# Kernel optimization log

Measured on AMD Instinct MI355X. Metric: run time of the kernel, lower is better.

Reference implementation:

```python
import jax, jax.numpy as jnp
import numpy as np

QMIN, QMAX = -128, 127  # signed int8 range


def setup_inputs() -> dict:
    key = jax.random.key(0)
    k_x, k_w, k_b = jax.random.split(key, 3)
    N, C_in, H, W = 32, 128, 56, 56
    C_out, kH, kW = 256, 3, 3
    # int8-valued tensors carried as int32 (jax-friendly); values in [-128, 127]
    x = jax.random.randint(k_x, (N, C_in, H, W), 0, 256, dtype=jnp.int32) - 128
    weight = jax.random.randint(k_w, (C_out, C_in, kH, kW), 0, 256, dtype=jnp.int32) - 128
    # int32 bias, already quantized with scale s_in * s_w
    bias = jax.random.randint(k_b, (C_out,), -(2 ** 14), 2 ** 14, dtype=jnp.int32)
    return {
        "x": x,
        "weight": weight,
        "bias": bias,
        "input_scale": jnp.float32(0.02),
        "weight_scale": jnp.float32(0.005),
        "output_scale": jnp.float32(0.05),
        "input_zero_point": jnp.int32(-5),
        "output_zero_point": jnp.int32(3),
    }


def reference(x, weight, bias, input_scale, weight_scale, output_scale,
              input_zero_point, output_zero_point):
    # Dequant-style integer conv: shift input by its zero point (weights are
    # symmetric, zero point 0), accumulate in fp32 (stands in for int32 acc).
    x_f = (x - input_zero_point).astype(jnp.float32)
    w_f = weight.astype(jnp.float32)
    acc = jax.lax.conv_general_dilated(
        x_f, w_f,
        window_strides=(1, 1),
        padding=((1, 1), (1, 1)),
        dimension_numbers=("NCHW", "OIHW", "NCHW"),
    )
    acc = acc + bias.astype(jnp.float32)[None, :, None, None]
    # Requantize: scale fusion + output zero point, round, clamp to int8.
    requant_scale = input_scale * weight_scale / output_scale
    y = acc * requant_scale + output_zero_point.astype(jnp.float32)
    y_q = jnp.clip(jnp.round(y), QMIN, QMAX).astype(jnp.int8)
    return y_q
```

## Files before the change

kernel.cpp:

```cpp
#include <hip/hip_runtime.h>
#include <stdint.h>


#define NB 32
#define CI 128
#define HH 56
#define WW 56
#define CO 256
#define SPA (HH * WW)
#define HP 58
#define WP 64
#define XP2_BYTES (NB * HP * WP * CI)
#define BP_BYTES (9 * 2 * 4 * CO * 16)

typedef int v4i __attribute__((ext_vector_type(4)));

__global__ __launch_bounds__(256) void prep_kernel(
    const int* __restrict__ x, const int* __restrict__ wgt,
    const int* __restrict__ bias, const int* __restrict__ zpi,
    int8_t* __restrict__ xp2, int8_t* __restrict__ bp, int* __restrict__ BG)
{
    __shared__ int sm[1824];
    const int tid = threadIdx.x, bid = blockIdx.x;
    const int zp = *zpi;
    const int zp4 = (zp & 255) * 0x01010101;

    if (bid < HH * NB) {
        const int n = bid / HH, h = bid % HH;
        #pragma unroll
        for (int it = 0; it < 7; ++it) {
            int j = tid + it * 256;
            int ci = j / 14, w4 = j - ci * 14;
            const v4i v = *(const v4i*)(x + ((n * CI + ci) * HH + h) * WW + w4 * 4);
            sm[w4 * 130 + ci] = (v.x & 255) | ((v.y & 255) << 8) |
                                ((v.z & 255) << 16) | (v.w << 24);
        }
        __syncthreads();
        int* od = (int*)xp2 + (n * HP + h + 1) * (WP * CI / 4);
        #pragma unroll
        for (int it = 0; it < 8; ++it) {
            int j = tid + it * 256;
            int widx = j >> 5, ci4 = j & 31;
            int val = zp4;
            if (widx >= 1 && widx <= WW) {
                int w = widx - 1;
                int base = (w >> 2) * 130 + ci4 * 4;
                int sh = (w & 3) * 8;
                val = ((sm[base] >> sh) & 0xff) | (((sm[base+1] >> sh) & 0xff) << 8) |
                      (((sm[base+2] >> sh) & 0xff) << 16) | ((sm[base+3] >> sh) << 24);
            }
            od[j ^ ((widx & 7) << 2)] = val;
        }
    } else if (bid < HH * NB + 2 * NB) {
        const int z = bid - HH * NB;
        const int n = z >> 1, hidx = (z & 1) ? (HP - 1) : 0;
        int* od = (int*)xp2 + (n * HP + hidx) * (WP * CI / 4);
        #pragma unroll
        for (int it = 0; it < 8; ++it) od[tid + it * 256] = zp4;
    } else {
        const int co = bid - (HH * NB + 2 * NB);
        for (int j = tid; j < 1152; j += 256) sm[j] = wgt[co * 1152 + j];
        __syncthreads();
        for (int j = tid; j < 288; j += 256) {
            int j4 = j & 3, q = (j >> 2) & 3, c64 = (j >> 4) & 1, t = j >> 5;
            int ci = c64 * 64 + q * 16 + j4 * 4;
            int b0 = sm[(ci + 0) * 9 + t] & 255, b1 = sm[(ci + 1) * 9 + t] & 255;
            int b2 = sm[(ci + 2) * 9 + t] & 255, b3 = sm[(ci + 3) * 9 + t];
            ((int*)bp)[((t * 2 + c64) * 4 + q) * 1024 + co * 4 + j4] =
                b0 | (b1 << 8) | (b2 << 16) | (b3 << 24);
        }
        if (tid < 9) {
            int s = 0;
            for (int ci = 0; ci < CI; ++ci) s += sm[ci * 9 + tid];
            sm[1152 + tid] = s;
        }
        __syncthreads();
        if (tid == 0) {
            int s9 = 0;
            for (int t = 0; t < 9; ++t) s9 += sm[1152 + t];
            BG[co] = bias[co] - zp * s9;
        }
    }
}

__global__ __launch_bounds__(256, 1) void qconv_mfma(
    const int8_t* __restrict__ xp2, const int8_t* __restrict__ bp,
    const int* __restrict__ BG,
    const float* __restrict__ si, const float* __restrict__ sw,
    const float* __restrict__ so, const int* __restrict__ zpo,
    int* __restrict__ out)
{
    const int tid  = threadIdx.x, lane = tid & 63, wid = tid >> 6;
    const int quad = lane >> 4, lo16 = lane & 15;
    const int bid  = blockIdx.x;
    const int x    = bid & 7, yb = bid >> 3;
    const int half = yb >> 4, coli = yb & 15;
    const int col  = x * 16 + coli;
    const int n = col >> 2, co64 = col & 3;
    const int cobase = co64 * 64;
    const int sfirst = half;
    const int ntiles = half ? 3 : 4;

    __shared__ __attribute__((aligned(16))) char smem[152 * 1024];
    char* Asm = smem;
    char* Bsm = smem + 80 * 1024;

    #pragma unroll
    for (int k = 0; k < 18; ++k) {
        const int u = wid + 4 * k;
        __builtin_amdgcn_global_load_lds(
            (const __attribute__((address_space(1))) void*)(bp + (u << 12) + cobase * 16 + lane * 16),
            (__attribute__((address_space(3))) void*)(Bsm + (u << 10)), 16, 0, 0);
    }
    const int8_t* aslab0 = xp2 + (((size_t)n * HP + sfirst * 8) << 13);
    #pragma unroll
    for (int k = 0; k < 20; ++k) {
        const int u = wid + 4 * k;
        __builtin_amdgcn_global_load_lds(
            (const __attribute__((address_space(1))) void*)(aslab0 + (u << 10) + lane * 16),
            (__attribute__((address_space(3))) void*)(Asm + (u << 10)), 16, 0, 0);
    }

    int abase[7];
    const int mw = wid * 112;
    #pragma unroll
    for (int mt = 0; mt < 7; ++mt) {
        const int ml = mw + mt * 16 + lo16;
        const int srow = ml / 56, scol = ml - srow * 56;
        abase[mt] = (srow * WP + scol) * 128 + quad * 16;
    }

    int bgv[4];
    #pragma unroll
    for (int ct = 0; ct < 4; ++ct) bgv[ct] = BG[cobase + ct * 16 + lo16];
    const float rs = (*si) * (*sw) / (*so);
    const float zo = (float)(*zpo);

    int* optr = out + (n * CO + cobase + lo16) * SPA + mw + quad * 4;

    __syncthreads();

    for (int tile = 0; tile < ntiles; ++tile) {
        const int slab = sfirst + 2 * tile;
        const int havenext = (tile + 1 < ntiles);

        v4i pre[20];
        if (havenext) {
            const int8_t* anext = xp2 + (((size_t)n * HP + (slab + 2) * 8) << 13);
            #pragma unroll
            for (int i = 0; i < 20; ++i)
                pre[i] = *(const v4i*)(anext + i * 4096 + tid * 16);
        }

        v4i acc[7][4];
        #pragma unroll
        for (int mt = 0; mt < 7; ++mt)
            #pragma unroll
            for (int ct = 0; ct < 4; ++ct) acc[mt][ct] = (v4i){0, 0, 0, 0};

        #pragma unroll
        for (int t = 0; t < 9; ++t) {
            const int toff = ((t / 3) * WP + (t % 3)) * 128;
            v4i b[2][4];
            #pragma unroll
            for (int c = 0; c < 2; ++c)
                #pragma unroll
                for (int ct = 0; ct < 4; ++ct)
                    b[c][ct] = *(const v4i*)(Bsm + ((t * 2 + c) * 4 + quad) * 1024 +
                                             lo16 * 16 + ct * 256);
            #pragma unroll
            for (int mt = 0; mt < 7; ++mt) {
                const int P = abase[mt] + toff;
                const int phys = P ^ (((P >> 7) & 7) << 4);
                v4i a0 = *(const v4i*)(Asm + phys);
                v4i a1 = *(const v4i*)(Asm + (phys ^ 64));
                #pragma unroll
                for (int ct = 0; ct < 4; ++ct)
                    acc[mt][ct] = __builtin_amdgcn_mfma_i32_16x16x64_i8(a0, b[0][ct], acc[mt][ct], 0, 0, 0);
                #pragma unroll
                for (int ct = 0; ct < 4; ++ct)
                    acc[mt][ct] = __builtin_amdgcn_mfma_i32_16x16x64_i8(a1, b[1][ct], acc[mt][ct], 0, 0, 0);
            }
        }

        __builtin_amdgcn_sched_barrier(0);
        __builtin_amdgcn_s_barrier();
        __builtin_amdgcn_sched_barrier(0);

        if (havenext) {
            #pragma unroll
            for (int i = 0; i < 20; ++i)
                *(v4i*)(Asm + i * 4096 + tid * 16) = pre[i];
        }

        const int sbase = slab * 448;
        #pragma unroll
        for (int mt = 0; mt < 7; ++mt) {
            #pragma unroll
            for (int ct = 0; ct < 4; ++ct) {
                v4i vv;
                #pragma unroll
                for (int i = 0; i < 4; ++i) {
                    float yv = rintf((float)(acc[mt][ct][i] + bgv[ct]) * rs + zo);
                    yv = fminf(fmaxf(yv, -128.f), 127.f);
                    vv[i] = (int)yv;
                }
                *(v4i*)(optr + sbase + ct * 16 * SPA + mt * 16) = vv;
            }
        }

        if (havenext) {
            asm volatile("s_waitcnt lgkmcnt(0)" ::: "memory");
            __builtin_amdgcn_sched_barrier(0);
            __builtin_amdgcn_s_barrier();
            __builtin_amdgcn_sched_barrier(0);
        }
    }
}

extern "C" void kernel_launch(void* const* d_in, const int* in_sizes, int n_in,
                              void* d_out, int out_size, void* d_ws, size_t ws_size,
                              hipStream_t stream) {
    const int*   x    = (const int*)d_in[0];
    const int*   wgt  = (const int*)d_in[1];
    const int*   bias = (const int*)d_in[2];
    const float* si   = (const float*)d_in[3];
    const float* sw   = (const float*)d_in[4];
    const float* so   = (const float*)d_in[5];
    const int*   zpi  = (const int*)d_in[6];
    const int*   zpo  = (const int*)d_in[7];
    int* out = (int*)d_out;

    int8_t* xp2 = (int8_t*)d_ws;
    int8_t* bp  = xp2 + XP2_BYTES;
    int*    bg  = (int*)(bp + BP_BYTES);

    prep_kernel<<<HH * NB + 2 * NB + CO, 256, 0, stream>>>(x, wgt, bias, zpi, xp2, bp, bg);
    qconv_mfma<<<256, 256, 0, stream>>>(xp2, bp, bg, si, sw, so, zpo, out);
}
```

Measured before the change: 196.8 us.

## Keep weights in registers, shrink A tiles, double-buffer LDS with async loads

Restructures the conv kernel so each wave keeps its 32-channel weight fragments resident in registers instead of re-reading them from LDS every tile. The workgroup splits into a 2x2 grid over spatial rows and output channels. It now processes seven 4-row slabs with a double-buffered LDS A tile, prefetched through global_load_lds, replacing register staging plus LDS stores. This removes LDS traffic for B and the register-to-LDS copy. The cost is heavy VGPR use (144 regs for weights) and a hand-tuned vmcnt wait whose correctness depends on the in-flight load count.

```diff
diff --git a/kernel.cpp b/kernel.cpp
--- a/kernel.cpp
+++ b/kernel.cpp
@@ -12,6 +12,7 @@
 #define WP 64
 #define XP2_BYTES (NB * HP * WP * CI)
 #define BP_BYTES (9 * 2 * 4 * CO * 16)
+#define ABUF (6 * 8192)
 
 typedef int v4i __attribute__((ext_vector_type(4)));
 
@@ -93,111 +94,99 @@
     const int tid  = threadIdx.x, lane = tid & 63, wid = tid >> 6;
     const int quad = lane >> 4, lo16 = lane & 15;
     const int bid  = blockIdx.x;
-    const int x    = bid & 7, yb = bid >> 3;
-    const int half = yb >> 4, coli = yb & 15;
-    const int col  = x * 16 + coli;
-    const int n = col >> 2, co64 = col & 3;
-    const int cobase = co64 * 64;
-    const int sfirst = half;
-    const int ntiles = half ? 3 : 4;
-
-    __shared__ __attribute__((aligned(16))) char smem[152 * 1024];
-    char* Asm = smem;
-    char* Bsm = smem + 80 * 1024;
-
-    #pragma unroll
-    for (int k = 0; k < 18; ++k) {
+    const int x    = bid & 7, r = bid >> 3;
+    const int n    = x * 4 + (r & 3);
+    const int co64 = (r >> 2) & 3;
+    const int p    = r >> 4;
+    const int mh   = wid >> 1, ch = wid & 1;
+    const int cw   = co64 * 64 + ch * 32;
+
+    __shared__ __attribute__((aligned(16))) int8_t Asm[2][ABUF];
+
+    const int8_t* src0 = xp2 + (((size_t)n * HP + 4 * p) << 13);
+    #pragma unroll
+    for (int k = 0; k < 12; ++k) {
         const int u = wid + 4 * k;
         __builtin_amdgcn_global_load_lds(
-            (const __attribute__((address_space(1))) void*)(bp + (u << 12) + cobase * 16 + lane * 16),
-            (__attribute__((address_space(3))) void*)(Bsm + (u << 10)), 16, 0, 0);
-    }
-    const int8_t* aslab0 = xp2 + (((size_t)n * HP + sfirst * 8) << 13);
-    #pragma unroll
-    for (int k = 0; k < 20; ++k) {
-        const int u = wid + 4 * k;
-        __builtin_amdgcn_global_load_lds(
-            (const __attribute__((address_space(1))) void*)(aslab0 + (u << 10) + lane * 16),
-            (__attribute__((address_space(3))) void*)(Asm + (u << 10)), 16, 0, 0);
-    }
-
-    int abase[7];
-    const int mw = wid * 112;
-    #pragma unroll
-    for (int mt = 0; mt < 7; ++mt) {
-        const int ml = mw + mt * 16 + lo16;
-        const int srow = ml / 56, scol = ml - srow * 56;
-        abase[mt] = (srow * WP + scol) * 128 + quad * 16;
-    }
-
-    int bgv[4];
-    #pragma unroll
-    for (int ct = 0; ct < 4; ++ct) bgv[ct] = BG[cobase + ct * 16 + lo16];
+            (const __attribute__((address_space(1))) void*)(src0 + (u << 10) + lane * 16),
+            (__attribute__((address_space(3))) void*)(&Asm[0][u << 10]), 16, 0, 0);
+    }
+
+    v4i breg[9][2][2];
+    #pragma unroll
+    for (int t = 0; t < 9; ++t)
+        #pragma unroll
+        for (int c = 0; c < 2; ++c)
+            #pragma unroll
+            for (int ct = 0; ct < 2; ++ct)
+                breg[t][c][ct] = *(const v4i*)(bp + (((t * 2 + c) * 4 + quad) << 12) +
+                                               (cw + ct * 16 + lo16) * 16);
+
+    int bgv[2];
+    #pragma unroll
+    for (int ct = 0; ct < 2; ++ct) bgv[ct] = BG[cw + ct * 16 + lo16];
     const float rs = (*si) * (*sw) / (*so);
     const float zo = (float)(*zpo);
 
-    int* optr = out + (n * CO + cobase + lo16) * SPA + mw + quad * 4;
+    int rowoff[7], colp[7][3];
+    #pragma unroll
+    for (int mt = 0; mt < 7; ++mt) {
+        const int ml = mh * 112 + mt * 16 + lo16;
+        const int srow = ml / 56, scol = ml - srow * 56;
+        rowoff[mt] = srow * 8192;
+        #pragma unroll
+        for (int dc = 0; dc < 3; ++dc) {
+            const int c2 = scol + dc;
+            colp[mt][dc] = (c2 * 128 + quad * 16) ^ ((c2 & 7) << 4);
+        }
+    }
 
     __syncthreads();
 
-    for (int tile = 0; tile < ntiles; ++tile) {
-        const int slab = sfirst + 2 * tile;
-        const int havenext = (tile + 1 < ntiles);
-
-        v4i pre[20];
-        if (havenext) {
-            const int8_t* anext = xp2 + (((size_t)n * HP + (slab + 2) * 8) << 13);
-            #pragma unroll
-            for (int i = 0; i < 20; ++i)
-                pre[i] = *(const v4i*)(anext + i * 4096 + tid * 16);
-        }
-
-        v4i acc[7][4];
+    #pragma unroll 1
+    for (int t7 = 0; t7 < 7; ++t7) {
+        const int s = p + 2 * t7;
+        const int8_t* curA = Asm[t7 & 1];
+
+        if (t7 < 6) {
+            const int8_t* srcn = xp2 + (((size_t)n * HP + 4 * (s + 2)) << 13);
+            int8_t* dst = (int8_t*)Asm[(t7 & 1) ^ 1];
+            #pragma unroll
+            for (int k = 0; k < 12; ++k) {
+                const int u = wid + 4 * k;
+                __builtin_amdgcn_global_load_lds(
+                    (const __attribute__((address_space(1))) void*)(srcn + (u << 10) + lane * 16),
+                    (__attribute__((address_space(3))) void*)(dst + (u << 10)), 16, 0, 0);
+            }
+        }
+        __builtin_amdgcn_sched_barrier(0);
+
+        v4i acc[7][2];
         #pragma unroll
         for (int mt = 0; mt < 7; ++mt)
             #pragma unroll
-            for (int ct = 0; ct < 4; ++ct) acc[mt][ct] = (v4i){0, 0, 0, 0};
-
-        #pragma unroll
-        for (int t = 0; t < 9; ++t) {
-            const int toff = ((t / 3) * WP + (t % 3)) * 128;
-            v4i b[2][4];
-            #pragma unroll
-            for (int c = 0; c < 2; ++c)
-                #pragma unroll
-                for (int ct = 0; ct < 4; ++ct)
-                    b[c][ct] = *(const v4i*)(Bsm + ((t * 2 + c) * 4 + quad) * 1024 +
-                                             lo16 * 16 + ct * 256);
+            for (int ct = 0; ct < 2; ++ct) acc[mt][ct] = (v4i){0, 0, 0, 0};
+
+        #pragma unroll
+        for (int tp = 0; tp < 9; ++tp) {
+            const int dr = tp / 3, dc = tp % 3;
             #pragma unroll
             for (int mt = 0; mt < 7; ++mt) {
-                const int P = abase[mt] + toff;
-                const int phys = P ^ (((P >> 7) & 7) << 4);
-                v4i a0 = *(const v4i*)(Asm + phys);
-                v4i a1 = *(const v4i*)(Asm + (phys ^ 64));
-                #pragma unroll
-                for (int ct = 0; ct < 4; ++ct)
-                    acc[mt][ct] = __builtin_amdgcn_mfma_i32_16x16x64_i8(a0, b[0][ct], acc[mt][ct], 0, 0, 0);
-                #pragma unroll
-                for (int ct = 0; ct < 4; ++ct)
-                    acc[mt][ct] = __builtin_amdgcn_mfma_i32_16x16x64_i8(a1, b[1][ct], acc[mt][ct], 0, 0, 0);
-            }
-        }
-
-        __builtin_amdgcn_sched_barrier(0);
-        __builtin_amdgcn_s_barrier();
-        __builtin_amdgcn_sched_barrier(0);
-
-        if (havenext) {
-            #pragma unroll
-            for (int i = 0; i < 20; ++i)
-                *(v4i*)(Asm + i * 4096 + tid * 16) = pre[i];
-        }
-
-        const int sbase = slab * 448;
+                const int off = rowoff[mt] + dr * 8192 + colp[mt][dc];
+                v4i a0 = *(const v4i*)(curA + off);
+                v4i a1 = *(const v4i*)(curA + (off ^ 64));
+                acc[mt][0] = __builtin_amdgcn_mfma_i32_16x16x64_i8(a0, breg[tp][0][0], acc[mt][0], 0, 0, 0);
+                acc[mt][1] = __builtin_amdgcn_mfma_i32_16x16x64_i8(a0, breg[tp][0][1], acc[mt][1], 0, 0, 0);
+                acc[mt][0] = __builtin_amdgcn_mfma_i32_16x16x64_i8(a1, breg[tp][1][0], acc[mt][0], 0, 0, 0);
+                acc[mt][1] = __builtin_amdgcn_mfma_i32_16x16x64_i8(a1, breg[tp][1][1], acc[mt][1], 0, 0, 0);
+            }
+        }
+
+        const int m0 = s * 224 + mh * 112;
         #pragma unroll
         for (int mt = 0; mt < 7; ++mt) {
             #pragma unroll
-            for (int ct = 0; ct < 4; ++ct) {
+            for (int ct = 0; ct < 2; ++ct) {
                 v4i vv;
                 #pragma unroll
                 for (int i = 0; i < 4; ++i) {
@@ -205,13 +194,14 @@
                     yv = fminf(fmaxf(yv, -128.f), 127.f);
                     vv[i] = (int)yv;
                 }
-                *(v4i*)(optr + sbase + ct * 16 * SPA + mt * 16) = vv;
-            }
-        }
-
-        if (havenext) {
-            asm volatile("s_waitcnt lgkmcnt(0)" ::: "memory");
+                *(v4i*)(out + (n * CO + cw + ct * 16 + lo16) * SPA +
+                        m0 + mt * 16 + quad * 4) = vv;
+            }
+        }
+
+        if (t7 < 6) {
             __builtin_amdgcn_sched_barrier(0);
+            asm volatile("s_waitcnt vmcnt(14)" ::: "memory");
             __builtin_amdgcn_s_barrier();
             __builtin_amdgcn_sched_barrier(0);
         }
```

New measurement: 187.4 us. -4.8%, faster.
